# Kernel optimization log

Measured on AMD Instinct MI355X. Metric: run time of the kernel, lower is better.

Reference implementation:

```python
import jax, jax.numpy as jnp
import numpy as np

E = 1024
H = 16
HD = E // H  # head_dim = 64
N, T, S = 2, 2048, 2048
NEG = -1e9


def setup_inputs() -> dict:
    key = jax.random.key(0)
    ks = jax.random.split(key, 12)
    s = 0.02
    inp = {
        "query": jax.random.normal(ks[0], (N, T, E), jnp.float32),
        "key": jax.random.normal(ks[1], (N, S, E), jnp.float32),
        "value": jax.random.normal(ks[2], (N, S, E), jnp.float32),
        # causal mask: mask[i, j] == 0 means target i cannot attend to source j
        "attn_mask": jnp.tril(jnp.ones((T, S), jnp.float32)),
        "pad_mask": jnp.zeros((N, S), bool),
        "Wq": jax.random.normal(ks[3], (E, E), jnp.float32) * s,
        "bq": jnp.zeros((E,), jnp.float32),
        "Wk": jax.random.normal(ks[4], (E, E), jnp.float32) * s,
        "bk": jnp.zeros((E,), jnp.float32),
        "Wv": jax.random.normal(ks[5], (E, E), jnp.float32) * s,
        "bv": jnp.zeros((E,), jnp.float32),
        "Wp": jax.random.normal(ks[6], (E, E), jnp.float32) * s,
        "bp": jnp.zeros((E,), jnp.float32),
    }
    return inp


def reference(query, key, value, attn_mask, pad_mask, Wq, bq, Wk, bk, Wv, bv, Wp, bp):
    n, t, _ = query.shape
    _, srcl, _ = key.shape
    # Linear projections (torch Linear: x @ W.T + b), split into heads
    Q = (query @ Wq.T + bq).reshape(n, t, H, HD).transpose(0, 2, 1, 3)      # (N,H,T,HD)
    K = (key @ Wk.T + bk).reshape(n, srcl, H, HD).transpose(0, 2, 1, 3)     # (N,H,S,HD)
    V = (value @ Wv.T + bv).reshape(n, srcl, H, HD).transpose(0, 2, 1, 3)   # (N,H,S,HD)
    scores = jnp.einsum("nhtd,nhsd->nhts", Q, K) / jnp.sqrt(jnp.float32(HD))
    scores = jnp.where(pad_mask[:, None, None, :], NEG, scores)
    scores = jnp.where(attn_mask[None, None, :, :] == 0, NEG, scores)
    att = jax.nn.softmax(scores, axis=-1)  # dropout=0 (eval)
    Y = jnp.einsum("nhts,nhsd->nhtd", att, V)
    Y = Y.transpose(0, 2, 1, 3).reshape(n, t, E)
    return Y @ Wp.T + bp
```

## Files before the change

### kernel.cpp

```cpp
#include <hip/hip_runtime.h>
#include <hip/hip_bf16.h>

#define E_  1024
#define H_  16
#define HD_ 64
#define NB  2
#define T_  2048
#define S_  2048
#define KD  1024

typedef __attribute__((ext_vector_type(8))) short short8;
typedef __attribute__((ext_vector_type(4))) short short4v;
typedef __attribute__((ext_vector_type(4))) float floatx4;

static __device__ __forceinline__ unsigned short f2bf(float f) {
    unsigned int u = __float_as_uint(f);
    unsigned int r = (u + 0x7FFFu + ((u >> 16) & 1u)) >> 16;
    return (unsigned short)r;
}

static __device__ __forceinline__ floatx4 mfma16(short8 a, short8 b, floatx4 c) {
    return __builtin_amdgcn_mfma_f32_16x16x32_bf16(a, b, c, 0, 0, 0);
}

static __device__ __forceinline__ void gload_lds16(const void* g, void* l) {
    __builtin_amdgcn_global_load_lds(
        (const __attribute__((address_space(1))) unsigned int*)g,
        (__attribute__((address_space(3))) unsigned int*)l, 16, 0, 0);
}

__global__ __launch_bounds__(256) void conv_all_kernel(
    const float* __restrict__ wq, const float* __restrict__ wk,
    const float* __restrict__ wv, const float* __restrict__ wp,
    const float* __restrict__ qi, const float* __restrict__ ki,
    const float* __restrict__ vi,
    unsigned short* __restrict__ Wb, unsigned short* __restrict__ Xb)
{
    const int NW4 = 1 << 18;
    const int NX4 = 1 << 20;
    const int TOT = 4 * NW4 + 3 * NX4;
    int idx = blockIdx.x * 256 + threadIdx.x;
    for (int i4 = idx; i4 < TOT; i4 += 262144) {
        const float* s; unsigned short* d; int off4;
        if (i4 < 4 * NW4) {
            int seg = i4 >> 18; off4 = i4 & (NW4 - 1);
            s = (seg == 0) ? wq : (seg == 1) ? wk : (seg == 2) ? wv : wp;
            d = Wb + ((size_t)seg << 20);
        } else {
            int j = i4 - 4 * NW4; int seg = j >> 20; off4 = j & (NX4 - 1);
            s = (seg == 0) ? qi : (seg == 1) ? ki : vi;
            d = Xb + ((size_t)seg << 22);
        }
        float4 v = *(const float4*)&s[(size_t)off4 * 4];
        short4v b;
        b[0] = (short)f2bf(v.x); b[1] = (short)f2bf(v.y);
        b[2] = (short)f2bf(v.z); b[3] = (short)f2bf(v.w);
        *(short4v*)&d[(size_t)off4 * 4] = b;
    }
}

__global__ __launch_bounds__(256) void proj_qkv_kernel(
    const unsigned short* __restrict__ Xb, const unsigned short* __restrict__ Wb,
    const float* __restrict__ bq, const float* __restrict__ bk, const float* __restrict__ bv,
    unsigned short* __restrict__ Qh, unsigned short* __restrict__ K2, unsigned short* __restrict__ V2)
{
    const int z = blockIdx.z;
    const unsigned short* X = Xb + ((size_t)z << 22);
    const unsigned short* W = Wb + ((size_t)z << 20);
    const float* bias = (z == 0) ? bq : (z == 1) ? bk : bv;
    unsigned short* dst = (z == 0) ? Qh : (z == 1) ? K2 : V2;

    __shared__ unsigned short Sm[16384];
    unsigned short* As = Sm;
    unsigned short* Bs = Sm + 8192;

    const int tid  = threadIdx.x;
    const int lane = tid & 63;
    const int w    = tid >> 6;
    const int wm   = w >> 1, wn = w & 1;
    const int m0   = blockIdx.x * 128;
    const int e0   = blockIdx.y * 128;
    const int l15  = lane & 15, lg = lane >> 4;

    floatx4 acc[4][4];
#pragma unroll
    for (int mi = 0; mi < 4; ++mi)
#pragma unroll
        for (int ni = 0; ni < 4; ++ni)
            acc[mi][ni] = (floatx4){0.f, 0.f, 0.f, 0.f};

    const int rc = lane >> 3;
    const int sl = (lane & 7) ^ rc;

    for (int kt = 0; kt < KD / 64; ++kt) {
        const int k0 = kt * 64;
#pragma unroll
        for (int jj = 0; jj < 4; ++jj) {
            int c = w * 4 + jj;
            int row = c * 8 + rc;
            gload_lds16(&X[(size_t)(m0 + row) * KD + k0 + sl * 8], &As[c * 512]);
            gload_lds16(&W[(size_t)(e0 + row) * KD + k0 + sl * 8], &Bs[c * 512]);
        }
        __syncthreads();

#pragma unroll
        for (int ks = 0; ks < 2; ++ks) {
            short8 af[4], bf[4];
#pragma unroll
            for (int mi = 0; mi < 4; ++mi) {
                int r_ = wm * 64 + mi * 16 + l15;
                af[mi] = *(const short8*)&As[r_ * 64 + (((ks * 4 + lg) ^ (r_ & 7)) << 3)];
            }
#pragma unroll
            for (int ni = 0; ni < 4; ++ni) {
                int r_ = wn * 64 + ni * 16 + l15;
                bf[ni] = *(const short8*)&Bs[r_ * 64 + (((ks * 4 + lg) ^ (r_ & 7)) << 3)];
            }
#pragma unroll
            for (int mi = 0; mi < 4; ++mi)
#pragma unroll
                for (int ni = 0; ni < 4; ++ni)
                    acc[mi][ni] = mfma16(af[mi], bf[ni], acc[mi][ni]);
        }
        __syncthreads();
    }

    if (z != 2) {
#pragma unroll
        for (int mi = 0; mi < 4; ++mi)
#pragma unroll
            for (int ni = 0; ni < 4; ++ni) {
                int col = wn * 64 + ni * 16 + l15;
                float bb = bias[e0 + col];
#pragma unroll
                for (int r = 0; r < 4; ++r) {
                    int row = wm * 64 + mi * 16 + (lg << 2) + r;
                    Sm[row * 128 + (col ^ ((row & 7) << 3))] =
                        f2bf(acc[mi][ni][r] + bb);
                }
            }
    } else {
#pragma unroll
        for (int mi = 0; mi < 4; ++mi)
#pragma unroll
            for (int ni = 0; ni < 4; ++ni) {
                int col = wn * 64 + ni * 16 + l15;
                float bb = bias[e0 + col];
                int rb = wm * 64 + mi * 16 + (lg << 2);
                short4v sv;
#pragma unroll
                for (int r = 0; r < 4; ++r) sv[r] = (short)f2bf(acc[mi][ni][r] + bb);
                *(short4v*)&Sm[col * 128 + (rb ^ ((col & 7) << 3))] = sv;
            }
    }
    __syncthreads();

    {
        const int r0 = tid >> 1;
        const int cb = (tid & 1) * 64;
#pragma unroll
        for (int j = 0; j < 8; ++j) {
            int c = cb + j * 8;
            short8 v = *(const short8*)&Sm[r0 * 128 + (c ^ ((r0 & 7) << 3))];
            if (z == 0) {
                int m = m0 + r0, nn = m >> 11, t = m & (T_ - 1);
                int e = e0 + c, hh = e >> 6, d = e & 63;
                size_t hb = (size_t)(nn * H_ + hh) * (T_ * HD_);
                *(short8*)&dst[hb + (size_t)t * HD_ + d] = v;
            } else if (z == 1) {
                int m = m0 + r0, nn = m >> 11, t = m & (T_ - 1);
                int e = e0 + c, hh = e >> 6, d = e & 63;
                size_t hb = (size_t)(nn * H_ + hh) * (T_ * HD_);
                *(short8*)&dst[hb + (t >> 6) * 4096 + (t & 63) * 64 +
                               (((d >> 3) ^ (t & 7)) << 3)] = v;
            } else {
                int e = e0 + r0, hh = e >> 6, d = e & 63;
                int m = m0 + c, nn = m >> 11, t = m & (T_ - 1);
                size_t hb = (size_t)(nn * H_ + hh) * (T_ * HD_);
                *(short8*)&dst[hb + (t >> 6) * 4096 + d * 64 +
                               ((((t >> 3) & 7) ^ (d & 7)) << 3)] = v;
            }
        }
    }
}

__global__ __launch_bounds__(256) void flash_attn_kernel(
    const unsigned short* __restrict__ Qh, const unsigned short* __restrict__ K2,
    const unsigned short* __restrict__ V2, unsigned short* __restrict__ Y)
{
    const int linear = blockIdx.x;
    const int nid = (linear & 7) * 64 + (linear >> 3);
    const int pb = nid & 15, h = (nid >> 4) & 15, n = nid >> 8;

    const int tid = threadIdx.x, lane = tid & 63, w = tid >> 6;
    const int l15 = lane & 15, lg = lane >> 4;

    const unsigned short* Qp = Qh + (size_t)(n * H_ + h) * (T_ * HD_);
    const unsigned short* Kt = K2 + (size_t)(n * H_ + h) * (T_ * HD_);
    const unsigned short* Vt = V2 + (size_t)(n * H_ + h) * (T_ * HD_);

    __shared__ unsigned short Ks_l[8192];
    __shared__ unsigned short VT_l[8192];
    __shared__ unsigned short Ps[64][136];

    const int prow = w * 16 + lg * 4;
    const int arow = w * 16 + l15;
    const int sw7  = l15 & 7;

#pragma unroll
    for (int side = 0; side < 2; ++side) {
        const int qt = side ? (31 - pb) : pb;
        const int q0 = qt * 64;
        const int nkv = (qt + 2) >> 1;

        short8 qf[2];
#pragma unroll
        for (int ks = 0; ks < 2; ++ks)
            qf[ks] = *(const short8*)&Qp[(size_t)(q0 + arow) * HD_ + ks * 32 + lg * 8];

        floatx4 o[4];
        float lacc[4];
#pragma unroll
        for (int hi = 0; hi < 4; ++hi) o[hi] = (floatx4){0.f, 0.f, 0.f, 0.f};
#pragma unroll
        for (int r = 0; r < 4; ++r) lacc[r] = 0.f;

        for (int kb2 = 0; kb2 < nkv; ++kb2) {
            __syncthreads();
            const unsigned short* Ksrc = Kt + kb2 * 8192;
            const unsigned short* Vsrc = Vt + kb2 * 8192;
#pragma unroll
            for (int j = 0; j < 4; ++j) {
                int c = w * 4 + j;
                gload_lds16(&Ksrc[c * 512 + lane * 8], &Ks_l[c * 512]);
                gload_lds16(&Vsrc[c * 512 + lane * 8], &VT_l[c * 512]);
            }
            __syncthreads();

            floatx4 sa[8];
#pragma unroll
            for (int ni = 0; ni < 8; ++ni) sa[ni] = (floatx4){0.f, 0.f, 0.f, 0.f};
            __builtin_amdgcn_s_setprio(1);
#pragma unroll
            for (int ks = 0; ks < 2; ++ks) {
                short8 kf[8];
#pragma unroll
                for (int ni = 0; ni < 8; ++ni)
                    kf[ni] = *(const short8*)
                        &Ks_l[(ni * 16 + l15) * 64 + (((ks * 4 + lg) ^ sw7) << 3)];
#pragma unroll
                for (int ni = 0; ni < 8; ++ni)
                    sa[ni] = mfma16(qf[ks], kf[ni], sa[ni]);
            }
            __builtin_amdgcn_s_setprio(0);

            const bool diag = (kb2 == nkv - 1);
            const int sbase = kb2 * 128;
            float pv[8][4];
#pragma unroll
            for (int ni = 0; ni < 8; ++ni)
#pragma unroll
                for (int r = 0; r < 4; ++r) {
                    float e = __expf(sa[ni][r] * 0.125f);
                    if (diag && (sbase + ni * 16 + l15 > q0 + prow + r)) e = 0.f;
                    pv[ni][r] = e;
                }
#pragma unroll
            for (int r = 0; r < 4; ++r)
                lacc[r] += ((pv[0][r] + pv[1][r]) + (pv[2][r] + pv[3][r]))
                         + ((pv[4][r] + pv[5][r]) + (pv[6][r] + pv[7][r]));

#pragma unroll
            for (int ni = 0; ni < 8; ++ni)
#pragma unroll
                for (int r = 0; r < 4; ++r)
                    Ps[prow + r][(ni * 16 + l15) ^ (lg << 3)] = f2bf(pv[ni][r]);

            __builtin_amdgcn_s_setprio(1);
#pragma unroll
            for (int ksp = 0; ksp < 4; ++ksp) {
                short8 pa = *(const short8*)
                    &Ps[arow][(ksp * 32 + lg * 8) ^ ((l15 >> 2) << 3)];
                short8 vt[4];
#pragma unroll
                for (int hi = 0; hi < 4; ++hi)
                    vt[hi] = *(const short8*)
                        &VT_l[(ksp >> 1) * 4096 + (hi * 16 + l15) * 64 +
                              ((((ksp & 1) * 4 + lg) ^ sw7) << 3)];
#pragma unroll
                for (int hi = 0; hi < 4; ++hi)
                    o[hi] = mfma16(pa, vt[hi], o[hi]);
            }
            __builtin_amdgcn_s_setprio(0);
        }

        float linv[4];
#pragma unroll
        for (int r = 0; r < 4; ++r) {
            float l = lacc[r];
#pragma unroll
            for (int off = 1; off < 16; off <<= 1)
                l += __shfl_xor(l, off);
            linv[r] = 1.0f / l;
        }

#pragma unroll
        for (int hi = 0; hi < 4; ++hi) {
            int col = hi * 16 + l15;
#pragma unroll
            for (int r = 0; r < 4; ++r) {
                int t = q0 + prow + r;
                Y[((size_t)n * T_ + t) * E_ + h * HD_ + col] =
                    f2bf(o[hi][r] * linv[r]);
            }
        }
    }
}

__global__ __launch_bounds__(256) void proj_out_kernel(
    const unsigned short* __restrict__ Yb, const unsigned short* __restrict__ Wpb,
    const float* __restrict__ bp, float* __restrict__ out)
{
    __shared__ unsigned short As[128 * 64];
    __shared__ unsigned short Bs[128 * 64];

    const int tid  = threadIdx.x;
    const int lane = tid & 63;
    const int w    = tid >> 6;
    const int wm   = w >> 1, wn = w & 1;
    const int m0   = blockIdx.x * 128;
    const int e0   = blockIdx.y * 128;
    const int l15  = lane & 15, lg = lane >> 4;

    floatx4 acc[4][4];
#pragma unroll
    for (int mi = 0; mi < 4; ++mi)
#pragma unroll
        for (int ni = 0; ni < 4; ++ni)
            acc[mi][ni] = (floatx4){0.f, 0.f, 0.f, 0.f};

    const int rc = lane >> 3;
    const int sl = (lane & 7) ^ rc;

    for (int kt = 0; kt < E_ / 64; ++kt) {
        const int k0 = kt * 64;
#pragma unroll
        for (int jj = 0; jj < 4; ++jj) {
            int c = w * 4 + jj;
            int row = c * 8 + rc;
            gload_lds16(&Yb[(size_t)(m0 + row) * E_ + k0 + sl * 8], &As[c * 512]);
            gload_lds16(&Wpb[(size_t)(e0 + row) * E_ + k0 + sl * 8], &Bs[c * 512]);
        }
        __syncthreads();

#pragma unroll
        for (int ks = 0; ks < 2; ++ks) {
            short8 af[4], bf[4];
#pragma unroll
            for (int mi = 0; mi < 4; ++mi) {
                int r_ = wm * 64 + mi * 16 + l15;
                af[mi] = *(const short8*)&As[r_ * 64 + (((ks * 4 + lg) ^ (r_ & 7)) << 3)];
            }
#pragma unroll
            for (int ni = 0; ni < 4; ++ni) {
                int r_ = wn * 64 + ni * 16 + l15;
                bf[ni] = *(const short8*)&Bs[r_ * 64 + (((ks * 4 + lg) ^ (r_ & 7)) << 3)];
            }
#pragma unroll
            for (int mi = 0; mi < 4; ++mi)
#pragma unroll
                for (int ni = 0; ni < 4; ++ni)
                    acc[mi][ni] = mfma16(af[mi], bf[ni], acc[mi][ni]);
        }
        __syncthreads();
    }

#pragma unroll
    for (int mi = 0; mi < 4; ++mi) {
#pragma unroll
        for (int ni = 0; ni < 4; ++ni) {
            int e = e0 + wn * 64 + ni * 16 + l15;
            float bb = bp[e];
#pragma unroll
            for (int r = 0; r < 4; ++r) {
                int m = m0 + wm * 64 + mi * 16 + (lg << 2) + r;
                out[(size_t)m * E_ + e] = acc[mi][ni][r] + bb;
            }
        }
    }
}

extern "C" void kernel_launch(void* const* d_in, const int* in_sizes, int n_in,
                              void* d_out, int out_size, void* d_ws, size_t ws_size,
                              hipStream_t stream) {
    const float* query = (const float*)d_in[0];
    const float* key_  = (const float*)d_in[1];
    const float* value = (const float*)d_in[2];
    const float* Wq = (const float*)d_in[5];
    const float* bq = (const float*)d_in[6];
    const float* Wk = (const float*)d_in[7];
    const float* bk = (const float*)d_in[8];
    const float* Wv = (const float*)d_in[9];
    const float* bv = (const float*)d_in[10];
    const float* Wp = (const float*)d_in[11];
    const float* bp = (const float*)d_in[12];
    float* out = (float*)d_out;

    const size_t P = (size_t)NB * H_ * T_ * HD_;
    unsigned short* Qh  = (unsigned short*)d_ws;
    unsigned short* K2  = Qh + P;
    unsigned short* V2  = K2 + P;
    unsigned short* Wb  = V2 + P;
    unsigned short* Xb  = Wb + (4u << 20);
    unsigned short* Yb  = Xb;
    unsigned short* Wpb = Wb + (3u << 20);

    conv_all_kernel<<<dim3(1024), 256, 0, stream>>>(
        Wq, Wk, Wv, Wp, query, key_, value, Wb, Xb);
    proj_qkv_kernel<<<dim3(32, 8, 3), 256, 0, stream>>>(
        Xb, Wb, bq, bk, bv, Qh, K2, V2);
    flash_attn_kernel<<<dim3(512), 256, 0, stream>>>(Qh, K2, V2, Yb);
    proj_out_kernel<<<dim3(32, 8), 256, 0, stream>>>(Yb, Wpb, bp, out);
}
```

Before: 127.3 us.

## Double-buffer LDS tiles in projection GEMMs to overlap loads with MFMA

Both the QKV projection and output projection GEMMs now use two LDS buffers per operand, prefetching the next K-tile through global_load_lds while MFMAs run on the current tile. The loads for the next tile are split across the two k-substeps, and each iteration ends with a single vmcnt(0) wait plus a barrier instead of two syncthreads. This is meant to hide global memory latency inside the compute. In exchange, LDS use per block doubles to 64KB, which may lower occupancy.

Result: faster. 115.0 us (-9.6%).

```diff
diff --git a/kernel.cpp b/kernel.cpp
--- a/kernel.cpp
+++ b/kernel.cpp
@@ -28,6 +28,13 @@
         (const __attribute__((address_space(1))) unsigned int*)g,
         (__attribute__((address_space(3))) unsigned int*)l, 16, 0, 0);
 }
+
+#define VMCNT0_BARRIER() do {                                   \
+    __builtin_amdgcn_sched_barrier(0);                          \
+    asm volatile("s_waitcnt vmcnt(0)" ::: "memory");            \
+    __builtin_amdgcn_s_barrier();                               \
+    __builtin_amdgcn_sched_barrier(0);                          \
+} while (0)
 
 __global__ __launch_bounds__(256) void conv_all_kernel(
     const float* __restrict__ wq, const float* __restrict__ wk,
@@ -70,9 +77,7 @@
     const float* bias = (z == 0) ? bq : (z == 1) ? bk : bv;
     unsigned short* dst = (z == 0) ? Qh : (z == 1) ? K2 : V2;
 
-    __shared__ unsigned short Sm[16384];
-    unsigned short* As = Sm;
-    unsigned short* Bs = Sm + 8192;
+    __shared__ unsigned short Sm[32768];
 
     const int tid  = threadIdx.x;
     const int lane = tid & 63;
@@ -92,29 +97,43 @@
     const int rc = lane >> 3;
     const int sl = (lane & 7) ^ rc;
 
-    for (int kt = 0; kt < KD / 64; ++kt) {
-        const int k0 = kt * 64;
-#pragma unroll
-        for (int jj = 0; jj < 4; ++jj) {
-            int c = w * 4 + jj;
-            int row = c * 8 + rc;
-            gload_lds16(&X[(size_t)(m0 + row) * KD + k0 + sl * 8], &As[c * 512]);
-            gload_lds16(&W[(size_t)(e0 + row) * KD + k0 + sl * 8], &Bs[c * 512]);
-        }
-        __syncthreads();
-
-#pragma unroll
-        for (int ks = 0; ks < 2; ++ks) {
+#pragma unroll
+    for (int jj = 0; jj < 4; ++jj) {
+        int c = w * 4 + jj;
+        int row = c * 8 + rc;
+        gload_lds16(&X[(size_t)(m0 + row) * KD + sl * 8], &Sm[c * 512]);
+        gload_lds16(&W[(size_t)(e0 + row) * KD + sl * 8], &Sm[16384 + c * 512]);
+    }
+    VMCNT0_BARRIER();
+
+    for (int kt = 0; kt < 16; ++kt) {
+        const int cur = (kt & 1) * 8192;
+        const int nxt = ((kt + 1) & 1) * 8192;
+        const unsigned short* Ac = Sm + cur;
+        const unsigned short* Bc = Sm + 16384 + cur;
+        unsigned short* An = Sm + nxt;
+        unsigned short* Bn = Sm + 16384 + nxt;
+        const int k0n = (kt + 1) * 64;
+
+        if (kt < 15) {
+#pragma unroll
+            for (int jj = 0; jj < 4; ++jj) {
+                int c = w * 4 + jj;
+                int row = c * 8 + rc;
+                gload_lds16(&X[(size_t)(m0 + row) * KD + k0n + sl * 8], &An[c * 512]);
+            }
+        }
+        {
             short8 af[4], bf[4];
 #pragma unroll
             for (int mi = 0; mi < 4; ++mi) {
                 int r_ = wm * 64 + mi * 16 + l15;
-                af[mi] = *(const short8*)&As[r_ * 64 + (((ks * 4 + lg) ^ (r_ & 7)) << 3)];
+                af[mi] = *(const short8*)&Ac[r_ * 64 + ((lg ^ (r_ & 7)) << 3)];
             }
 #pragma unroll
             for (int ni = 0; ni < 4; ++ni) {
                 int r_ = wn * 64 + ni * 16 + l15;
-                bf[ni] = *(const short8*)&Bs[r_ * 64 + (((ks * 4 + lg) ^ (r_ & 7)) << 3)];
+                bf[ni] = *(const short8*)&Bc[r_ * 64 + ((lg ^ (r_ & 7)) << 3)];
             }
 #pragma unroll
             for (int mi = 0; mi < 4; ++mi)
@@ -122,7 +141,33 @@
                 for (int ni = 0; ni < 4; ++ni)
                     acc[mi][ni] = mfma16(af[mi], bf[ni], acc[mi][ni]);
         }
-        __syncthreads();
+        if (kt < 15) {
+#pragma unroll
+            for (int jj = 0; jj < 4; ++jj) {
+                int c = w * 4 + jj;
+                int row = c * 8 + rc;
+                gload_lds16(&W[(size_t)(e0 + row) * KD + k0n + sl * 8], &Bn[c * 512]);
+            }
+        }
+        {
+            short8 af[4], bf[4];
+#pragma unroll
+            for (int mi = 0; mi < 4; ++mi) {
+                int r_ = wm * 64 + mi * 16 + l15;
+                af[mi] = *(const short8*)&Ac[r_ * 64 + (((4 + lg) ^ (r_ & 7)) << 3)];
+            }
+#pragma unroll
+            for (int ni = 0; ni < 4; ++ni) {
+                int r_ = wn * 64 + ni * 16 + l15;
+                bf[ni] = *(const short8*)&Bc[r_ * 64 + (((4 + lg) ^ (r_ & 7)) << 3)];
+            }
+#pragma unroll
+            for (int mi = 0; mi < 4; ++mi)
+#pragma unroll
+                for (int ni = 0; ni < 4; ++ni)
+                    acc[mi][ni] = mfma16(af[mi], bf[ni], acc[mi][ni]);
+        }
+        VMCNT0_BARRIER();
     }
 
     if (z != 2) {
@@ -321,8 +366,7 @@
     const unsigned short* __restrict__ Yb, const unsigned short* __restrict__ Wpb,
     const float* __restrict__ bp, float* __restrict__ out)
 {
-    __shared__ unsigned short As[128 * 64];
-    __shared__ unsigned short Bs[128 * 64];
+    __shared__ unsigned short Sm[32768];
 
     const int tid  = threadIdx.x;
     const int lane = tid & 63;
@@ -342,29 +386,43 @@
     const int rc = lane >> 3;
     const int sl = (lane & 7) ^ rc;
 
-    for (int kt = 0; kt < E_ / 64; ++kt) {
-        const int k0 = kt * 64;
-#pragma unroll
-        for (int jj = 0; jj < 4; ++jj) {
-            int c = w * 4 + jj;
-            int row = c * 8 + rc;
-            gload_lds16(&Yb[(size_t)(m0 + row) * E_ + k0 + sl * 8], &As[c * 512]);
-            gload_lds16(&Wpb[(size_t)(e0 + row) * E_ + k0 + sl * 8], &Bs[c * 512]);
-        }
-        __syncthreads();
-
-#pragma unroll
-        for (int ks = 0; ks < 2; ++ks) {
+#pragma unroll
+    for (int jj = 0; jj < 4; ++jj) {
+        int c = w * 4 + jj;
+        int row = c * 8 + rc;
+        gload_lds16(&Yb[(size_t)(m0 + row) * E_ + sl * 8], &Sm[c * 512]);
+        gload_lds16(&Wpb[(size_t)(e0 + row) * E_ + sl * 8], &Sm[16384 + c * 512]);
+    }
+    VMCNT0_BARRIER();
+
+    for (int kt = 0; kt < 16; ++kt) {
+        const int cur = (kt & 1) * 8192;
+        const int nxt = ((kt + 1) & 1) * 8192;
+        const unsigned short* Ac = Sm + cur;
+        const unsigned short* Bc = Sm + 16384 + cur;
+        unsigned short* An = Sm + nxt;
+        unsigned short* Bn = Sm + 16384 + nxt;
+        const int k0n = (kt + 1) * 64;
+
+        if (kt < 15) {
+#pragma unroll
+            for (int jj = 0; jj < 4; ++jj) {
+                int c = w * 4 + jj;
+                int row = c * 8 + rc;
+                gload_lds16(&Yb[(size_t)(m0 + row) * E_ + k0n + sl * 8], &An[c * 512]);
+            }
+        }
+        {
             short8 af[4], bf[4];
 #pragma unroll
             for (int mi = 0; mi < 4; ++mi) {
                 int r_ = wm * 64 + mi * 16 + l15;
-                af[mi] = *(const short8*)&As[r_ * 64 + (((ks * 4 + lg) ^ (r_ & 7)) << 3)];
+                af[mi] = *(const short8*)&Ac[r_ * 64 + ((lg ^ (r_ & 7)) << 3)];
             }
 #pragma unroll
             for (int ni = 0; ni < 4; ++ni) {
                 int r_ = wn * 64 + ni * 16 + l15;
-                bf[ni] = *(const short8*)&Bs[r_ * 64 + (((ks * 4 + lg) ^ (r_ & 7)) << 3)];
+                bf[ni] = *(const short8*)&Bc[r_ * 64 + ((lg ^ (r_ & 7)) << 3)];
             }
 #pragma unroll
             for (int mi = 0; mi < 4; ++mi)
@@ -372,7 +430,33 @@
                 for (int ni = 0; ni < 4; ++ni)
                     acc[mi][ni] = mfma16(af[mi], bf[ni], acc[mi][ni]);
         }
-        __syncthreads();
+        if (kt < 15) {
+#pragma unroll
+            for (int jj = 0; jj < 4; ++jj) {
+                int c = w * 4 + jj;
+                int row = c * 8 + rc;
+                gload_lds16(&Wpb[(size_t)(e0 + row) * E_ + k0n + sl * 8], &Bn[c * 512]);
+            }
+        }
+        {
+            short8 af[4], bf[4];
+#pragma unroll
+            for (int mi = 0; mi < 4; ++mi) {
+                int r_ = wm * 64 + mi * 16 + l15;
+                af[mi] = *(const short8*)&Ac[r_ * 64 + (((4 + lg) ^ (r_ & 7)) << 3)];
+            }
+#pragma unroll
+            for (int ni = 0; ni < 4; ++ni) {
+                int r_ = wn * 64 + ni * 16 + l15;
+                bf[ni] = *(const short8*)&Bc[r_ * 64 + (((4 + lg) ^ (r_ & 7)) << 3)];
+            }
+#pragma unroll
+            for (int mi = 0; mi < 4; ++mi)
+#pragma unroll
+                for (int ni = 0; ni < 4; ++ni)
+                    acc[mi][ni] = mfma16(af[mi], bf[ni], acc[mi][ni]);
+        }
+        VMCNT0_BARRIER();
     }
 
 #pragma unroll
```
